# Performance work log

Measured on AMD Instinct MI355X. Metric: run time of the kernel, lower is better.

## Reference

```python
import jax, jax.numpy as jnp
import numpy as np

B, T, V, E, H, HD, L, K = 64, 512, 50000, 512, 512, 256, 2, 16
START, STOP, PAD = 13, 14, 15
NEG = -10000.0


def setup_inputs() -> dict:
    key = jax.random.key(0)
    ks = jax.random.split(key, 12)
    x = jax.random.randint(ks[0], (B, T), 0, V, dtype=jnp.int32)
    emb_table = jax.random.normal(ks[1], (V, E), jnp.float32) * 0.1
    w_ih = jax.random.normal(ks[2], (L, 2, 4 * HD, E), jnp.float32) * 0.05
    w_hh = jax.random.normal(ks[3], (L, 2, 4 * HD, HD), jnp.float32) * 0.05
    b_ih = jax.random.normal(ks[4], (L, 2, 4 * HD), jnp.float32) * 0.05
    b_hh = jax.random.normal(ks[5], (L, 2, 4 * HD), jnp.float32) * 0.05
    h0 = jax.random.normal(ks[6], (2 * L, B, HD), jnp.float32)
    c0 = jax.random.normal(ks[7], (2 * L, B, HD), jnp.float32)
    w_out = jax.random.normal(ks[8], (K, H), jnp.float32) * 0.05
    b_out = jax.random.normal(ks[9], (K,), jnp.float32) * 0.05
    t = jax.random.normal(ks[10], (K, K), jnp.float32)
    # replicate the in-place edits (order matters: pad overrides stop/start crossings)
    t = t.at[START, :].set(NEG)
    t = t.at[:, STOP].set(NEG)
    t = t.at[PAD, :].set(0.0)
    t = t.at[:, PAD].set(0.0)
    return {"x": x, "seq_len": T, "emb_table": emb_table, "w_ih": w_ih,
            "w_hh": w_hh, "b_ih": b_ih, "b_hh": b_hh, "h0": h0, "c0": c0,
            "w_out": w_out, "b_out": b_out, "transition": t}


def _lstm_dir(xs, h0, c0, Wih, Whh, b):
    # xs: [B, T, in]; single-direction LSTM, torch gate order (i, f, g, o)
    def step(carry, x_t):
        h, c = carry
        gates = x_t @ Wih.T + h @ Whh.T + b  # [B, 4*HD]
        i, f, g, o = jnp.split(gates, 4, axis=-1)
        c = jax.nn.sigmoid(f) * c + jax.nn.sigmoid(i) * jnp.tanh(g)
        h = jax.nn.sigmoid(o) * jnp.tanh(c)
        return (h, c), h
    _, hs = jax.lax.scan(step, (h0, c0), jnp.swapaxes(xs, 0, 1))  # [T, B, HD]
    return jnp.swapaxes(hs, 0, 1)


def _log_exp_sum(vec):
    # faithful to the original: per-row max over last dim, but sum of exp over ALL elements
    m = jnp.max(vec, axis=-1)
    return m + jnp.log(jnp.sum(jnp.exp(vec - m[..., None])))


def reference(x, seq_len, emb_table, w_ih, w_hh, b_ih, b_hh, h0, c0, w_out, b_out, transition):
    out = emb_table[x]  # [B, T, E]
    for l in range(L):
        fwd = _lstm_dir(out, h0[2 * l], c0[2 * l], w_ih[l, 0], w_hh[l, 0], b_ih[l, 0] + b_hh[l, 0])
        bwd = _lstm_dir(out[:, ::-1], h0[2 * l + 1], c0[2 * l + 1], w_ih[l, 1], w_hh[l, 1], b_ih[l, 1] + b_hh[l, 1])[:, ::-1]
        out = jnp.concatenate([fwd, bwd], axis=-1)  # [B, T, H]
    tag_scores = out @ w_out.T + b_out  # [B, T, K]

    # CRF forward algorithm (vectorized form of the nested time/tag loops)
    alpha0 = jnp.full((B, K), NEG, dtype=tag_scores.dtype).at[:, START].set(0.0)

    def crf_step(alpha, feat_t):  # feat_t: [B, K]
        vec = alpha[:, None, :] + feat_t[:, :, None] + transition[None, :, :]  # [B, Knext, Kprev]
        m = jnp.max(vec, axis=-1)  # [B, Knext]
        # original log_exp_sum sums exp over the whole [B, Kprev] slice per next_tag
        s = jnp.sum(jnp.exp(vec - m[..., None]), axis=(0, 2))  # [Knext]
        return m + jnp.log(s)[None, :], None

    alpha, _ = jax.lax.scan(crf_step, alpha0, jnp.swapaxes(tag_scores, 0, 1))
    terminal = alpha + transition[STOP][None, :]
    forward_score = _log_exp_sum(terminal)  # [B]
    return tag_scores, forward_score
```

## Files before the change

kernel.cpp:

```cpp
#include <hip/hip_runtime.h>

#define B_ 64
#define T_ 512
#define E_ 512
#define HD_ 256
#define H_ 512
#define K_ 16
#define NEG_ (-10000.0f)
#define START_ 13
#define STOP_ 14

typedef unsigned int u32;
using half8  = __attribute__((ext_vector_type(8))) _Float16;
using f32x4  = __attribute__((ext_vector_type(4))) float;
using half2v = __attribute__((ext_vector_type(2))) _Float16;

__device__ __forceinline__ int dot4i8(u32 a, u32 b, int c) {
#if __has_builtin(__builtin_amdgcn_sdot4)
    return __builtin_amdgcn_sdot4((int)a, (int)b, c, false);
#else
    int r = c;
#pragma unroll
    for (int i = 0; i < 4; ++i) {
        int xa = ((int)a << (24 - 8 * i)) >> 24;
        int xb = ((int)b << (24 - 8 * i)) >> 24;
        r += xa * xb;
    }
    return r;
#endif
}
__device__ __forceinline__ int dotq(uint4 w, uint4 h, int a) {
    a = dot4i8(w.x, h.x, a); a = dot4i8(w.y, h.y, a);
    a = dot4i8(w.z, h.z, a); a = dot4i8(w.w, h.w, a);
    return a;
}
__device__ __forceinline__ float sigm(float x) { return 1.f / (1.f + __expf(-x)); }
__device__ __forceinline__ float tanh_f(float x) {
    float a = fabsf(x);
    float e = __expf(-2.f * a);
    float t = (1.f - e) / (1.f + e);
    return x < 0.f ? -t : t;
}

__device__ __forceinline__ float wave_sum64(float x) {
#if __has_builtin(__builtin_amdgcn_update_dpp)
#define DPPADD_(ctrl)                                                                  \
    x += __builtin_bit_cast(float, __builtin_amdgcn_update_dpp(                        \
             0, __builtin_bit_cast(int, x), ctrl, 0xf, 0xf, true))
    DPPADD_(0x111); DPPADD_(0x112); DPPADD_(0x114); DPPADD_(0x118);
    DPPADD_(0x142); DPPADD_(0x143);
#undef DPPADD_
    return __builtin_bit_cast(float, __builtin_amdgcn_readlane(__builtin_bit_cast(int, x), 63));
#else
#pragma unroll
    for (int off = 32; off >= 1; off >>= 1) x += __shfl_xor(x, off, 64);
    return x;
#endif
}

__global__ void cvt_f16_k(const float* __restrict__ src, _Float16* __restrict__ dst, int n4) {
    int i = blockIdx.x * blockDim.x + threadIdx.x;
    if (i < n4) {
        float4 v = ((const float4*)src)[i];
        half2v a; a.x = (_Float16)v.x; a.y = (_Float16)v.y;
        half2v b; b.x = (_Float16)v.z; b.y = (_Float16)v.w;
        ((u32*)dst)[2 * i]     = __builtin_bit_cast(u32, a);
        ((u32*)dst)[2 * i + 1] = __builtin_bit_cast(u32, b);
    }
}
__global__ void bias_sum_k(const float* __restrict__ bih, const float* __restrict__ bhh,
                           float* __restrict__ bs) {
    int i = blockIdx.x * blockDim.x + threadIdx.x;
    if (i < 4096) bs[i] = bih[i] + bhh[i];
}

__global__ void quant_whh_k(const float* __restrict__ whh,
                            u32* __restrict__ wq,
                            float* __restrict__ dqw) {
    const int row = blockIdx.x, lane = threadIdx.x;
    const float4 v = ((const float4*)(whh + (size_t)row * 256))[lane];
    float m = fmaxf(fmaxf(fabsf(v.x), fabsf(v.y)), fmaxf(fabsf(v.z), fabsf(v.w)));
#pragma unroll
    for (int off = 32; off >= 1; off >>= 1) m = fmaxf(m, __shfl_xor(m, off, 64));
    m = fmaxf(m, 1e-8f);
    const float s = 127.f / m;
    int b0 = ((int)rintf(v.x * s)) & 255;
    int b1 = ((int)rintf(v.y * s)) & 255;
    int b2 = ((int)rintf(v.z * s)) & 255;
    int b3 = ((int)rintf(v.w * s)) & 255;
    wq[(size_t)row * 64 + lane] = (u32)(b0 | (b1 << 8) | (b2 << 16) | (b3 << 24));
    if (lane == 0) dqw[row] = m / (127.f * 127.f);
}

__global__ void embed_k(const int* __restrict__ x, const float* __restrict__ emb,
                        _Float16* __restrict__ xe) {
    int m = blockIdx.x;
    int row = x[m];
    int c = threadIdx.x * 4;
    float4 v = *(const float4*)(emb + (size_t)row * E_ + c);
    half2v p0; p0.x = (_Float16)v.x; p0.y = (_Float16)v.y;
    half2v p1; p1.x = (_Float16)v.z; p1.y = (_Float16)v.w;
    u32* dst = (u32*)(xe + (size_t)m * E_) + threadIdx.x * 2;
    dst[0] = __builtin_bit_cast(u32, p0);
    dst[1] = __builtin_bit_cast(u32, p1);
}

__global__ __launch_bounds__(256) void gemm_bt(const _Float16* __restrict__ A,
                                               const _Float16* __restrict__ Bw,
                                               const float* __restrict__ bsum,
                                               _Float16* __restrict__ C,
                                               int M, int N, int Kd) {
    __shared__ __align__(16) _Float16 As[128 * 64];
    __shared__ __align__(16) _Float16 Bs[128 * 64];
    const int nTn = N >> 7;
    const int nwg = gridDim.x;
    const int idx = (blockIdx.x & 7) * (nwg >> 3) + (blockIdx.x >> 3);
    const int tm = idx / nTn, tn = idx % nTn;
    const int tid = threadIdx.x;
    const int lane = tid & 63, wave = tid >> 6;
    const int wr = wave >> 1, wc = wave & 1;
    f32x4 acc[4][4];
#pragma unroll
    for (int i = 0; i < 4; ++i)
#pragma unroll
        for (int j = 0; j < 4; ++j) acc[i][j] = f32x4{0.f, 0.f, 0.f, 0.f};
    const int lr = lane & 15, lk = (lane >> 4) * 8;

    for (int k0 = 0; k0 < Kd; k0 += 64) {
#pragma unroll
        for (int r = 0; r < 4; ++r) {
            int c = r * 256 + tid;
            const _Float16* srcA = A + (size_t)(tm * 128 + (c >> 3)) * Kd + k0 + (c & 7) * 8;
            const _Float16* srcB = Bw + (size_t)(tn * 128 + (c >> 3)) * Kd + k0 + (c & 7) * 8;
            _Float16* dA = &As[(size_t)(r * 256 + wave * 64) * 8];
            _Float16* dB = &Bs[(size_t)(r * 256 + wave * 64) * 8];
            __builtin_amdgcn_global_load_lds((const __attribute__((address_space(1))) void*)srcA,
                                             (__attribute__((address_space(3))) void*)dA, 16, 0, 0);
            __builtin_amdgcn_global_load_lds((const __attribute__((address_space(1))) void*)srcB,
                                             (__attribute__((address_space(3))) void*)dB, 16, 0, 0);
        }
        __syncthreads();
#pragma unroll
        for (int kk = 0; kk < 2; ++kk) {
            half8 av[4], bv[4];
#pragma unroll
            for (int i = 0; i < 4; ++i)
                av[i] = *(const half8*)&As[(wr * 64 + i * 16 + lr) * 64 + kk * 32 + lk];
#pragma unroll
            for (int j = 0; j < 4; ++j)
                bv[j] = *(const half8*)&Bs[(wc * 64 + j * 16 + lr) * 64 + kk * 32 + lk];
#pragma unroll
            for (int i = 0; i < 4; ++i)
#pragma unroll
                for (int j = 0; j < 4; ++j)
                    acc[i][j] = __builtin_amdgcn_mfma_f32_16x16x32_f16(av[i], bv[j], acc[i][j], 0, 0, 0);
        }
        __syncthreads();
    }
    const int mq = (lane >> 4) * 4;
#pragma unroll
    for (int i = 0; i < 4; ++i)
#pragma unroll
        for (int j = 0; j < 4; ++j) {
            int m0 = tm * 128 + wr * 64 + i * 16 + mq;
            int n0 = tn * 128 + wc * 64 + j * 16 + lr;
            float bv = bsum[n0];
#pragma unroll
            for (int q = 0; q < 4; ++q)
                C[(size_t)(m0 + q) * N + n0] = (_Float16)(acc[i][j][q] + bv);
        }
}

__global__ __attribute__((amdgpu_flat_work_group_size(512, 512), amdgpu_waves_per_eu(2, 2)))
void lstm_layer_k(
    const u32* __restrict__ wq,
    const float* __restrict__ dqw,
    const float* __restrict__ h0,
    const float* __restrict__ c0,
    const _Float16* __restrict__ Z,
    _Float16* __restrict__ Hout) {
    __shared__ __align__(16) u32 hbuf[2][64];
    __shared__ float g_sh[1024];
    __shared__ float m0sh;
    const int tid = threadIdx.x;
    const int b = blockIdx.x >> 1, dir = blockIdx.x & 1;
    const int R0 = tid, R1 = tid + 512;

    const uint4* w4 = (const uint4*)(wq + (size_t)dir * 1024 * 64);
    uint4 wa[16], wb[16];
#pragma unroll
    for (int i = 0; i < 16; ++i) wa[i] = w4[(size_t)R0 * 16 + i];
#pragma unroll
    for (int i = 0; i < 16; ++i) wb[i] = w4[(size_t)R1 * 16 + i];
#pragma unroll
    for (int i = 0; i < 16; ++i) {
        asm volatile("" : "+v"(wa[i].x), "+v"(wa[i].y), "+v"(wa[i].z), "+v"(wa[i].w));
        asm volatile("" : "+v"(wb[i].x), "+v"(wb[i].y), "+v"(wb[i].z), "+v"(wb[i].w));
    }
    const float dq0 = dqw[dir * 1024 + R0];
    const float dq1 = dqw[dir * 1024 + R1];

    float c = 0.f;
    if (tid < 256) c = c0[(size_t)dir * B_ * HD_ + b * HD_ + tid];
    if (tid < 64) {
        float4 hv = ((const float4*)(h0 + (size_t)dir * B_ * HD_ + (size_t)b * HD_))[tid];
        float am = fmaxf(fmaxf(fabsf(hv.x), fabsf(hv.y)), fmaxf(fabsf(hv.z), fabsf(hv.w)));
#pragma unroll
        for (int off = 32; off >= 1; off >>= 1) am = fmaxf(am, __shfl_xor(am, off, 64));
        am = fmaxf(am, 1e-6f);
        float sc = 127.f / am;
        int q0 = ((int)rintf(hv.x * sc)) & 255, q1 = ((int)rintf(hv.y * sc)) & 255;
        int q2 = ((int)rintf(hv.z * sc)) & 255, q3 = ((int)rintf(hv.w * sc)) & 255;
        hbuf[0][tid] = (u32)(q0 | (q1 << 8) | (q2 << 16) | (q3 << 24));
        if (tid == 0) m0sh = am;
    }
    const _Float16* Zr = Z + (size_t)b * T_ * 2048 + dir * 1024;
    const int t0 = dir ? (T_ - 1) : 0;
    float z0 = (float)Zr[(size_t)t0 * 2048 + R0];
    float z1 = (float)Zr[(size_t)t0 * 2048 + R1];
    __syncthreads();
    const float m0v = m0sh;

    for (int s = 0; s < T_; ++s) {
        const int t = dir ? (T_ - 1 - s) : s;
        float zn0 = 0.f, zn1 = 0.f;
        if (s + 1 < T_) {
            const int tn = dir ? (t - 1) : (t + 1);
            zn0 = (float)Zr[(size_t)tn * 2048 + R0];
            zn1 = (float)Zr[(size_t)tn * 2048 + R1];
        }
        const uint4* hb = (const uint4*)&hbuf[s & 1][0];
        int a0 = 0, a1 = 0;
#pragma unroll
        for (int i = 0; i < 16; ++i) {
            uint4 hv = hb[i];
            a0 = dotq(wa[i], hv, a0);
            a1 = dotq(wb[i], hv, a1);
        }
        const float sc = (s == 0) ? m0v : 1.f;
        g_sh[R0] = (float)a0 * (dq0 * sc) + z0;
        g_sh[R1] = (float)a1 * (dq1 * sc) + z1;
        z0 = zn0; z1 = zn1;
        __syncthreads();
        if (tid < 256) {
            float gi = g_sh[tid], gf = g_sh[tid + 256];
            float gg = g_sh[tid + 512], go = g_sh[tid + 768];
            c = sigm(gf) * c + sigm(gi) * tanh_f(gg);
            float h = sigm(go) * tanh_f(c);
            Hout[(size_t)(b * T_ + t) * H_ + dir * HD_ + tid] = (_Float16)h;
            ((signed char*)&hbuf[(s + 1) & 1][0])[tid] = (signed char)(int)rintf(h * 127.f);
        }
        __syncthreads();
    }
}

__global__ __launch_bounds__(256) void tag_k(const _Float16* __restrict__ Hs,
                                             const float* __restrict__ wout,
                                             const float* __restrict__ bout,
                                             float* __restrict__ out) {
    const int tid = threadIdx.x;
    const int mi = tid >> 4, kk = tid & 15;
    const int m = blockIdx.x * 16 + mi;
    const uint4* hrow = (const uint4*)(Hs + (size_t)m * H_);
    const float4* wrow = (const float4*)(wout + (size_t)kk * H_);
    float acc = 0.f;
#pragma unroll 8
    for (int i = 0; i < 64; ++i) {
        uint4 hv = hrow[i];
        float4 w0 = wrow[2 * i], w1 = wrow[2 * i + 1];
        half2v p0 = __builtin_bit_cast(half2v, hv.x), p1 = __builtin_bit_cast(half2v, hv.y);
        half2v p2 = __builtin_bit_cast(half2v, hv.z), p3 = __builtin_bit_cast(half2v, hv.w);
        acc += (float)p0.x * w0.x + (float)p0.y * w0.y + (float)p1.x * w0.z + (float)p1.y * w0.w
             + (float)p2.x * w1.x + (float)p2.y * w1.y + (float)p3.x * w1.z + (float)p3.y * w1.w;
    }
    out[(size_t)m * K_ + kk] = acc + bout[kk];
}

__global__ __launch_bounds__(1024) void crf_k(const float* __restrict__ tag,
                                              const float* __restrict__ trans,
                                              float* __restrict__ out) {
    __shared__ __align__(16) float albuf[2][64][20];
    const int tid = threadIdx.x;
    const int kn = tid >> 6, b = tid & 63;
    float trow[16];
#pragma unroll
    for (int kp = 0; kp < 16; ++kp) trow[kp] = trans[kn * 16 + kp];
    if (kn < 2) {
    }
    albuf[0][b][kn] = (kn == START_) ? 0.f : NEG_;
    __syncthreads();
    const float* tagb = tag + (size_t)b * T_ * K_ + kn;
    float featc = tagb[0];
    int cur = 0;
    for (int t = 0; t < T_; ++t) {
        float featn = 0.f;
        if (t + 1 < T_) featn = tagb[(size_t)(t + 1) * K_];
        float4 a0 = *(const float4*)&albuf[cur][b][0];
        float4 a1 = *(const float4*)&albuf[cur][b][4];
        float4 a2 = *(const float4*)&albuf[cur][b][8];
        float4 a3 = *(const float4*)&albuf[cur][b][12];
        float v[16];
        v[0] = a0.x + trow[0];  v[1] = a0.y + trow[1];  v[2] = a0.z + trow[2];  v[3] = a0.w + trow[3];
        v[4] = a1.x + trow[4];  v[5] = a1.y + trow[5];  v[6] = a1.z + trow[6];  v[7] = a1.w + trow[7];
        v[8] = a2.x + trow[8];  v[9] = a2.y + trow[9];  v[10] = a2.z + trow[10]; v[11] = a2.w + trow[11];
        v[12] = a3.x + trow[12]; v[13] = a3.y + trow[13]; v[14] = a3.z + trow[14]; v[15] = a3.w + trow[15];
        float m = v[0];
#pragma unroll
        for (int kp = 1; kp < 16; ++kp) m = fmaxf(m, v[kp]);
        float sm = 0.f;
#pragma unroll
        for (int kp = 0; kp < 16; ++kp) sm += __expf(v[kp] - m);
        sm = wave_sum64(sm);
        albuf[cur ^ 1][b][kn] = featc + m + __logf(sm);
        featc = featn;
        __syncthreads();
        cur ^= 1;
    }
    const float term = albuf[cur][b][kn] + trans[STOP_ * 16 + kn];
    albuf[cur ^ 1][b][kn] = term;
    __syncthreads();
    if (tid < 64) {
        float mb = -3.4e38f;
#pragma unroll
        for (int k2 = 0; k2 < 16; ++k2) mb = fmaxf(mb, albuf[cur ^ 1][tid][k2]);
        float p = 0.f;
#pragma unroll
        for (int k2 = 0; k2 < 16; ++k2) p += __expf(albuf[cur ^ 1][tid][k2] - mb);
#pragma unroll
        for (int off = 32; off >= 1; off >>= 1) p += __shfl_xor(p, off, 64);
        out[(size_t)B_ * T_ * K_ + tid] = mb + __logf(p);
    }
}

extern "C" void kernel_launch(void* const* d_in, const int* in_sizes, int n_in,
                              void* d_out, int out_size, void* d_ws, size_t ws_size,
                              hipStream_t stream) {
    const int*   x     = (const int*)d_in[0];
    const float* emb   = (const float*)d_in[2];
    const float* w_ih  = (const float*)d_in[3];
    const float* w_hh  = (const float*)d_in[4];
    const float* b_ih  = (const float*)d_in[5];
    const float* b_hh  = (const float*)d_in[6];
    const float* h0    = (const float*)d_in[7];
    const float* c0    = (const float*)d_in[8];
    const float* w_out = (const float*)d_in[9];
    const float* b_out = (const float*)d_in[10];
    const float* trans = (const float*)d_in[11];
    float* out = (float*)d_out;

    char* ws = (char*)d_ws;
    u32*      wq    = (u32*)ws;
    float*    dqw   = (float*)(ws + ((size_t)1 << 20));
    _Float16* wih16 = (_Float16*)(ws + ((size_t)2 << 20));
    float*    bsum  = (float*)(ws + ((size_t)6 << 20));
    _Float16* xe    = (_Float16*)(ws + ((size_t)7 << 20));
    _Float16* Zb    = (_Float16*)(ws + ((size_t)39 << 20));
    _Float16* H0b   = (_Float16*)(ws + ((size_t)167 << 20));
    if (ws_size < ((size_t)199 << 20)) return;

    quant_whh_k<<<4096, 64, 0, stream>>>(w_hh, wq, dqw);
    cvt_f16_k<<<2048, 256, 0, stream>>>(w_ih, wih16, 2097152 / 4);
    bias_sum_k<<<16, 256, 0, stream>>>(b_ih, b_hh, bsum);
    embed_k<<<B_ * T_, 128, 0, stream>>>(x, emb, xe);

    gemm_bt<<<(32768 / 128) * (2048 / 128), 256, 0, stream>>>(xe, wih16, bsum, Zb, 32768, 2048, 512);
    lstm_layer_k<<<128, 512, 0, stream>>>(wq, dqw, h0, c0, Zb, H0b);
    gemm_bt<<<(32768 / 128) * (2048 / 128), 256, 0, stream>>>(H0b, wih16 + (size_t)2048 * 512, bsum + 2048, Zb, 32768, 2048, 512);
    lstm_layer_k<<<128, 512, 0, stream>>>(wq + (size_t)2048 * 64, dqw + 2048,
                                          h0 + 2 * B_ * HD_, c0 + 2 * B_ * HD_, Zb, xe );
    tag_k<<<32768 / 16, 256, 0, stream>>>(xe, w_out, b_out, out);
    crf_k<<<1, 1024, 0, stream>>>(out, trans, out);
}
```

Baseline: 1.880 ms.

## Remap LSTM gate rows so lane pairs exchange gates via DPP, dropping one barrier

Gate rows are reassigned so each pair of adjacent lanes holds the i/f/g/o pre-activations for one hidden unit. The halves are swapped with a DPP quad-perm instead of a shared-memory round trip, and every thread computes the cell update redundantly. This removes the gate scratch buffer and one __syncthreads per timestep in the recurrent loop. The cost is duplicated sigmoid/tanh work across all 512 threads and scattered weight-row loads at setup.

```diff
diff --git a/kernel.cpp b/kernel.cpp
--- a/kernel.cpp
+++ b/kernel.cpp
@@ -40,6 +40,15 @@
     float e = __expf(-2.f * a);
     float t = (1.f - e) / (1.f + e);
     return x < 0.f ? -t : t;
+}
+
+__device__ __forceinline__ float pair_swap(float x) {
+#if __has_builtin(__builtin_amdgcn_update_dpp)
+    return __builtin_bit_cast(float, __builtin_amdgcn_update_dpp(
+               0, __builtin_bit_cast(int, x), 0xB1, 0xf, 0xf, true));
+#else
+    return __shfl_xor(x, 1, 64);
+#endif
 }
 
 __device__ __forceinline__ float wave_sum64(float x) {
@@ -180,11 +189,12 @@
     const _Float16* __restrict__ Z,
     _Float16* __restrict__ Hout) {
     __shared__ __align__(16) u32 hbuf[2][64];
-    __shared__ float g_sh[1024];
     __shared__ float m0sh;
     const int tid = threadIdx.x;
     const int b = blockIdx.x >> 1, dir = blockIdx.x & 1;
-    const int R0 = tid, R1 = tid + 512;
+    const int k = tid >> 1, p = tid & 1;
+    const int R0 = p * 256 + k;
+    const int R1 = 512 + p * 256 + k;
 
     const uint4* w4 = (const uint4*)(wq + (size_t)dir * 1024 * 64);
     uint4 wa[16], wb[16];
@@ -200,8 +210,7 @@
     const float dq0 = dqw[dir * 1024 + R0];
     const float dq1 = dqw[dir * 1024 + R1];
 
-    float c = 0.f;
-    if (tid < 256) c = c0[(size_t)dir * B_ * HD_ + b * HD_ + tid];
+    float c = c0[(size_t)dir * B_ * HD_ + b * HD_ + k];
     if (tid < 64) {
         float4 hv = ((const float4*)(h0 + (size_t)dir * B_ * HD_ + (size_t)b * HD_))[tid];
         float am = fmaxf(fmaxf(fabsf(hv.x), fabsf(hv.y)), fmaxf(fabsf(hv.z), fabsf(hv.w)));
@@ -220,6 +229,7 @@
     float z1 = (float)Zr[(size_t)t0 * 2048 + R1];
     __syncthreads();
     const float m0v = m0sh;
+    float dqa = dq0 * m0v, dqb = dq1 * m0v;
 
     for (int s = 0; s < T_; ++s) {
         const int t = dir ? (T_ - 1 - s) : s;
@@ -237,19 +247,22 @@
             a0 = dotq(wa[i], hv, a0);
             a1 = dotq(wb[i], hv, a1);
         }
-        const float sc = (s == 0) ? m0v : 1.f;
-        g_sh[R0] = (float)a0 * (dq0 * sc) + z0;
-        g_sh[R1] = (float)a1 * (dq1 * sc) + z1;
+        float f0 = (float)a0 * dqa + z0;
+        float f1 = (float)a1 * dqb + z1;
+        float o0 = pair_swap(f0);
+        float o1 = pair_swap(f1);
+        float gi = p ? o0 : f0;
+        float gf = p ? f0 : o0;
+        float gg = p ? o1 : f1;
+        float go = p ? f1 : o1;
+        c = sigm(gf) * c + sigm(gi) * tanh_f(gg);
+        const float h = sigm(go) * tanh_f(c);
+        if (p == 0) {
+            Hout[(size_t)(b * T_ + t) * H_ + dir * HD_ + k] = (_Float16)h;
+            ((signed char*)&hbuf[(s + 1) & 1][0])[k] = (signed char)(int)rintf(h * 127.f);
+        }
+        if (s == 0) { dqa = dq0; dqb = dq1; }
         z0 = zn0; z1 = zn1;
-        __syncthreads();
-        if (tid < 256) {
-            float gi = g_sh[tid], gf = g_sh[tid + 256];
-            float gg = g_sh[tid + 512], go = g_sh[tid + 768];
-            c = sigm(gf) * c + sigm(gi) * tanh_f(gg);
-            float h = sigm(go) * tanh_f(c);
-            Hout[(size_t)(b * T_ + t) * H_ + dir * HD_ + tid] = (_Float16)h;
-            ((signed char*)&hbuf[(s + 1) & 1][0])[tid] = (signed char)(int)rintf(h * 127.f);
-        }
         __syncthreads();
     }
 }
@@ -285,8 +298,6 @@
     float trow[16];
 #pragma unroll
     for (int kp = 0; kp < 16; ++kp) trow[kp] = trans[kn * 16 + kp];
-    if (kn < 2) {
-    }
     albuf[0][b][kn] = (kn == START_) ? 0.f : NEG_;
     __syncthreads();
     const float* tagb = tag + (size_t)b * T_ * K_ + kn;
```

After: 1.972 ms. 1.05x slower.
